# Performance work log

Hardware: AMD Instinct MI355X
Metric: run time of the kernel (lower is better)

## Reference

```python
import jax, jax.numpy as jnp
import numpy as np

DIM = 384
HEADS = 12
W = 7  # window_size
N = W * W
B = 4096

def _relative_position_index(ws):
    ch = np.arange(ws)
    coords = np.stack(np.meshgrid(ch, ch, indexing='ij'))  # [2, W, W]
    cf = coords.reshape(2, -1)  # [2, W*W]
    rel = cf[:, :, None] - cf[:, None, :]  # [2, N, N]
    rel = rel.transpose(1, 2, 0)
    rel[:, :, 0] += ws - 1
    rel[:, :, 1] += ws - 1
    rel[:, :, 0] *= 2 * ws - 1
    return rel.sum(-1).astype(np.int32)  # [N, N]

def setup_inputs() -> dict:
    key = jax.random.key(0)
    ks = jax.random.split(key, 8)
    s = 0.02
    return {
        'x': jax.random.normal(ks[0], (B, N, DIM), jnp.float32),
        'y': jax.random.normal(ks[1], (B, N, DIM), jnp.float32),
        'q_w': jax.random.normal(ks[2], (DIM, DIM), jnp.float32) * s,
        'q_b': jnp.zeros((DIM,), jnp.float32),
        'kv_w': jax.random.normal(ks[3], (2 * DIM, DIM), jnp.float32) * s,
        'kv_b': jnp.zeros((2 * DIM,), jnp.float32),
        'proj_w': jax.random.normal(ks[4], (DIM, DIM), jnp.float32) * s,
        'proj_b': jnp.zeros((DIM,), jnp.float32),
        'rel_table': jax.random.normal(ks[5], ((2 * W - 1) ** 2, HEADS), jnp.float32) * s,
        'rel_index': jnp.asarray(_relative_position_index(W)),
    }

def reference(x, y, q_w, q_b, kv_w, kv_b, proj_w, proj_b, rel_table, rel_index):
    Bx, N1, C = x.shape
    N2 = y.shape[1]
    hd = C // HEADS
    scale = hd ** -0.5
    # projections (torch Linear: x @ W^T + b)
    q = (x @ q_w.T + q_b).reshape(Bx, N1, HEADS, hd)
    kv = (y @ kv_w.T + kv_b).reshape(Bx, N2, 2, HEADS, hd)
    k = kv[:, :, 0]  # [B, N2, H, d]
    v = kv[:, :, 1]
    attn = jnp.einsum('bqhd,bkhd->bhqk', q, k) * scale
    # relative position bias: [N1, N2, H] -> [H, N1, N2]
    bias = rel_table[rel_index.reshape(-1)].reshape(N1, N2, HEADS)
    attn = attn + jnp.transpose(bias, (2, 0, 1))[None]
    attn = jax.nn.softmax(attn, axis=-1)
    out = jnp.einsum('bhqk,bkhd->bqhd', attn, v).reshape(Bx, N1, C)
    return out @ proj_w.T + proj_b
```

## Files before the change

kernel.cpp:

```cpp
#include <hip/hip_runtime.h>

#define DIM 384
#define HEADS 12
#define HD 32
#define NTOK 49
#define NWIN 4096
#define MTOT (NWIN*NTOK)
#define PSTR 72

typedef __attribute__((ext_vector_type(8))) __bf16 bf16x8;
typedef __attribute__((ext_vector_type(4))) float f32x4;

static __device__ __forceinline__ f32x4 mfma16(bf16x8 a, bf16x8 b, f32x4 c) {
  return __builtin_amdgcn_mfma_f32_16x16x32_bf16(a, b, c, 0, 0, 0);
}

static __device__ __forceinline__ void gload_lds16(const void* g, void* l) {
  __builtin_amdgcn_global_load_lds(
      (const __attribute__((address_space(1))) unsigned int*)g,
      (__attribute__((address_space(3))) unsigned int*)l, 16, 0, 0);
}

__global__ void k_prep(const float* __restrict__ qw, const float* __restrict__ kvw,
                       const float* __restrict__ pw, const float* __restrict__ rel_table,
                       const int* __restrict__ rel_index,
                       __bf16* __restrict__ qw_bf, __bf16* __restrict__ kvw_bf,
                       __bf16* __restrict__ pw_bf, float* __restrict__ bias_pad) {
  int i = blockIdx.x * 256 + threadIdx.x;
  if (i < DIM*DIM)   qw_bf[i] = (__bf16)qw[i];
  if (i < 2*DIM*DIM) kvw_bf[i] = (__bf16)kvw[i];
  if (i < DIM*DIM)   pw_bf[i] = (__bf16)pw[i];
  if (i < HEADS*64*64) {
    int h = i >> 12, rem = i & 4095, q = rem >> 6, k = rem & 63;
    float v;
    if (k >= NTOK)      v = -1e30f;
    else if (q >= NTOK) v = 0.0f;
    else v = rel_table[rel_index[q*NTOK + k] * HEADS + h];
    bias_pad[i] = v;
  }
}

__global__ __launch_bounds__(256) void k_qkv(
    const float* __restrict__ x, const float* __restrict__ y,
    const __bf16* __restrict__ qw_bf, const __bf16* __restrict__ kvw_bf,
    const float* __restrict__ q_b, const float* __restrict__ kv_b,
    __bf16* __restrict__ Qws, __bf16* __restrict__ Kws, __bf16* __restrict__ Vws)
{
  int b = blockIdx.x;
  int orig = (b & 7) * 1764 + (b >> 3);
  int mtile = orig / 9;
  int nt9 = orig - mtile*9;
  const float* A; const __bf16* Bw; const float* bias; __bf16* Cout;
  int wrow0, col0;
  if (nt9 < 3) { A = x; Bw = qw_bf; bias = q_b; Cout = Qws; wrow0 = nt9*128; col0 = wrow0; }
  else {
    A = y; Bw = kvw_bf; bias = kv_b; wrow0 = (nt9-3)*128;
    if (wrow0 < DIM) { Cout = Kws; col0 = wrow0; } else { Cout = Vws; col0 = wrow0 - DIM; }
  }
  bias += wrow0;

  __shared__ __align__(16) float  As[2][128*32];
  __shared__ __align__(16) __bf16 Bs[2][128*32];

  int t = threadIdx.x;
  int lane = t & 63, wave = t >> 6;
  int l15 = lane & 15, g = lane >> 4;
  int wr = (wave >> 1) * 64, wc = (wave & 1) * 64;
  int row0b = mtile*128;

  const float* asrc[4];
  #pragma unroll
  for (int i = 0; i < 4; ++i)
    asrc[i] = A + (size_t)(row0b + i*32 + wave*8 + (lane>>3))*DIM
                + (((lane&7) ^ (lane>>3)) << 2);
  const __bf16* bsrc[2];
  #pragma unroll
  for (int i = 0; i < 2; ++i)
    bsrc[i] = Bw + (size_t)(wrow0 + i*64 + wave*16 + (lane>>2))*DIM
                 + (((lane&3) ^ ((lane>>2)&3)) << 3);

  f32x4 acc[4][4];
  #pragma unroll
  for (int a=0;a<4;a++)
    #pragma unroll
    for (int bb=0;bb<4;bb++) acc[a][bb] = (f32x4){0.f,0.f,0.f,0.f};

  #pragma unroll
  for (int i = 0; i < 4; ++i)
    gload_lds16(asrc[i], (char*)&As[0][0] + i*4096 + wave*1024);
  #pragma unroll
  for (int i = 0; i < 2; ++i)
    gload_lds16(bsrc[i], (char*)&Bs[0][0] + i*4096 + wave*1024);
  __syncthreads();

  int buf = 0;
  for (int kt = 0; kt < 12; ++kt) {
    if (kt < 11) {
      int kk = (kt+1)*32;
      #pragma unroll
      for (int i = 0; i < 4; ++i)
        gload_lds16(asrc[i] + kk, (char*)&As[buf^1][0] + i*4096 + wave*1024);
      #pragma unroll
      for (int i = 0; i < 2; ++i)
        gload_lds16(bsrc[i] + kk, (char*)&Bs[buf^1][0] + i*4096 + wave*1024);
    }
    bf16x8 af[4], bfv[4];
    #pragma unroll
    for (int a=0;a<4;a++) {
      int r = wr + a*16 + l15;
      const char* rowp = (const char*)&As[buf][0] + r*128;
      float4 v0 = *(const float4*)(rowp + ((((g<<1)  ) ^ (r&7)) << 4));
      float4 v1 = *(const float4*)(rowp + ((((g<<1)|1) ^ (r&7)) << 4));
      bf16x8 tt;
      tt[0]=(__bf16)v0.x; tt[1]=(__bf16)v0.y; tt[2]=(__bf16)v0.z; tt[3]=(__bf16)v0.w;
      tt[4]=(__bf16)v1.x; tt[5]=(__bf16)v1.y; tt[6]=(__bf16)v1.z; tt[7]=(__bf16)v1.w;
      af[a] = tt;
    }
    #pragma unroll
    for (int bb=0;bb<4;bb++) {
      int r = wc + bb*16 + l15;
      bfv[bb] = *(const bf16x8*)((const char*)&Bs[buf][0] + r*64 + ((g ^ (r&3)) << 4));
    }
    #pragma unroll
    for (int a=0;a<4;a++)
      #pragma unroll
      for (int bb=0;bb<4;bb++)
        acc[a][bb] = mfma16(af[a], bfv[bb], acc[a][bb]);
    __syncthreads();
    buf ^= 1;
  }

  #pragma unroll
  for (int a=0;a<4;a++) {
    #pragma unroll
    for (int bb=0;bb<4;bb++) {
      int colw = wc + bb*16 + l15;
      float bi = bias[colw];
      size_t cbase = (size_t)(row0b + wr + a*16 + 4*g)*DIM + (col0 + colw);
      #pragma unroll
      for (int r=0;r<4;r++)
        Cout[cbase + (size_t)r*DIM] = (__bf16)(acc[a][bb][r] + bi);
    }
  }
}

__global__ __launch_bounds__(256) void k_attn(
    __bf16* qao,
    const __bf16* __restrict__ Kws, const __bf16* __restrict__ Vws,
    const float* __restrict__ bias_pad)
{
  __shared__ __align__(16) __bf16 Psh[4][64*PSTR];
  __shared__ __align__(16) __bf16 VTsh[4][32*PSTR];
  int b = blockIdx.x;
  int lane = threadIdx.x & 63, wave = threadIdx.x >> 6;
  int l15 = lane & 15, g = lane >> 4;
  __bf16* Pw  = Psh[wave];
  __bf16* VTw = VTsh[wave];
  size_t rowbase = (size_t)b * NTOK * DIM;
  const float scale = 0.17677669529663687f;

  for (int e = lane; e < 32*15; e += 64) {
    int d = e / 15, k = 49 + (e - d*15);
    VTw[d*PSTR + k] = (__bf16)0.0f;
  }

  for (int hh = 0; hh < 3; hh++) {
    int h = wave + hh*4;
    for (int e = lane; e < NTOK*HD; e += 64) {
      int k = e >> 5, d = e & 31;
      VTw[d*PSTR + k] = Vws[rowbase + (size_t)k*DIM + h*HD + d];
    }
    bf16x8 qf[4], kf[4];
    #pragma unroll
    for (int mt=0; mt<4; mt++) {
      int q = 16*mt + l15; if (q > 48) q = 48;
      qf[mt] = *(const bf16x8*)(qao + rowbase + (size_t)q*DIM + h*HD + g*8);
    }
    #pragma unroll
    for (int nt=0; nt<4; nt++) {
      int kk = 16*nt + l15; if (kk > 48) kk = 48;
      kf[nt] = *(const bf16x8*)(Kws + rowbase + (size_t)kk*DIM + h*HD + g*8);
    }
    f32x4 sacc[4][4];
    #pragma unroll
    for (int mt=0; mt<4; mt++)
      #pragma unroll
      for (int nt=0; nt<4; nt++)
        sacc[mt][nt] = mfma16(qf[mt], kf[nt], (f32x4){0.f,0.f,0.f,0.f});

    const float* bt = bias_pad + h*4096;
    float rs[4][4];
    #pragma unroll
    for (int mt=0; mt<4; mt++) {
      #pragma unroll
      for (int r=0; r<4; r++) {
        int q = 16*mt + 4*g + r;
        float v0 = sacc[mt][0][r]*scale + bt[q*64 +  0 + l15];
        float v1 = sacc[mt][1][r]*scale + bt[q*64 + 16 + l15];
        float v2 = sacc[mt][2][r]*scale + bt[q*64 + 32 + l15];
        float v3 = sacc[mt][3][r]*scale + bt[q*64 + 48 + l15];
        float m = fmaxf(fmaxf(v0,v1), fmaxf(v2,v3));
        #pragma unroll
        for (int off=1; off<16; off<<=1) m = fmaxf(m, __shfl_xor(m, off));
        v0 = __expf(v0-m); v1 = __expf(v1-m); v2 = __expf(v2-m); v3 = __expf(v3-m);
        float s = v0+v1+v2+v3;
        #pragma unroll
        for (int off=1; off<16; off<<=1) s += __shfl_xor(s, off);
        rs[mt][r] = s;
        Pw[q*PSTR +  0 + l15] = (__bf16)v0;
        Pw[q*PSTR + 16 + l15] = (__bf16)v1;
        Pw[q*PSTR + 32 + l15] = (__bf16)v2;
        Pw[q*PSTR + 48 + l15] = (__bf16)v3;
      }
    }

    #pragma unroll
    for (int mt=0; mt<4; mt++) {
      #pragma unroll
      for (int dt=0; dt<2; dt++) {
        f32x4 o = (f32x4){0.f,0.f,0.f,0.f};
        #pragma unroll
        for (int ks=0; ks<2; ks++) {
          bf16x8 pa = *(const bf16x8*)(Pw  + (16*mt + l15)*PSTR + 32*ks + 8*g);
          bf16x8 vb = *(const bf16x8*)(VTw + (16*dt + l15)*PSTR + 32*ks + 8*g);
          o = mfma16(pa, vb, o);
        }
        #pragma unroll
        for (int r=0; r<4; r++) {
          int q = 16*mt + 4*g + r;
          if (q < NTOK)
            qao[rowbase + (size_t)q*DIM + h*HD + 16*dt + l15] = (__bf16)(o[r] / rs[mt][r]);
        }
      }
    }
  }
}

__global__ __launch_bounds__(256) void k_proj(
    const __bf16* __restrict__ Aao, const __bf16* __restrict__ pw_bf,
    const float* __restrict__ pb, float* __restrict__ out)
{
  int b = blockIdx.x;
  int orig = (b & 7) * 588 + (b >> 3);
  int mtile = orig / 3;
  int nt = orig - mtile*3;
  int lane = threadIdx.x & 63, wave = threadIdx.x >> 6;
  int l15 = lane & 15, g = lane >> 4;
  int wr = (wave >> 1) * 64, wc = (wave & 1) * 64;
  int row0b = mtile*128;
  int col00 = nt*128;

  __shared__ __align__(16) __bf16 As[2][128*32];
  __shared__ __align__(16) __bf16 Bs[2][128*32];

  const __bf16* asrc[2];
  const __bf16* bsrc[2];
  #pragma unroll
  for (int i = 0; i < 2; ++i) {
    asrc[i] = Aao   + (size_t)(row0b + i*64 + wave*16 + (lane>>2))*DIM
                    + (((lane&3) ^ ((lane>>2)&3)) << 3);
    bsrc[i] = pw_bf + (size_t)(col00 + i*64 + wave*16 + (lane>>2))*DIM
                    + (((lane&3) ^ ((lane>>2)&3)) << 3);
  }

  f32x4 acc[4][4];
  #pragma unroll
  for (int a=0;a<4;a++)
    #pragma unroll
    for (int bb=0;bb<4;bb++) acc[a][bb] = (f32x4){0.f,0.f,0.f,0.f};

  #pragma unroll
  for (int i = 0; i < 2; ++i) {
    gload_lds16(asrc[i], (char*)&As[0][0] + i*4096 + wave*1024);
    gload_lds16(bsrc[i], (char*)&Bs[0][0] + i*4096 + wave*1024);
  }
  __syncthreads();

  int buf = 0;
  for (int kt = 0; kt < 12; ++kt) {
    if (kt < 11) {
      int kk = (kt+1)*32;
      #pragma unroll
      for (int i = 0; i < 2; ++i) {
        gload_lds16(asrc[i] + kk, (char*)&As[buf^1][0] + i*4096 + wave*1024);
        gload_lds16(bsrc[i] + kk, (char*)&Bs[buf^1][0] + i*4096 + wave*1024);
      }
    }
    bf16x8 af[4], bfv[4];
    #pragma unroll
    for (int a=0;a<4;a++) {
      int r = wr + a*16 + l15;
      af[a] = *(const bf16x8*)((const char*)&As[buf][0] + r*64 + ((g ^ (r&3)) << 4));
    }
    #pragma unroll
    for (int bb=0;bb<4;bb++) {
      int r = wc + bb*16 + l15;
      bfv[bb] = *(const bf16x8*)((const char*)&Bs[buf][0] + r*64 + ((g ^ (r&3)) << 4));
    }
    #pragma unroll
    for (int a=0;a<4;a++)
      #pragma unroll
      for (int bb=0;bb<4;bb++)
        acc[a][bb] = mfma16(af[a], bfv[bb], acc[a][bb]);
    __syncthreads();
    buf ^= 1;
  }

  #pragma unroll
  for (int a=0;a<4;a++) {
    #pragma unroll
    for (int bb=0;bb<4;bb++) {
      int col = col00 + wc + bb*16 + l15;
      float bi = pb[col];
      size_t cbase = (size_t)(row0b + wr + a*16 + 4*g)*DIM + col;
      #pragma unroll
      for (int r=0;r<4;r++)
        out[cbase + (size_t)r*DIM] = acc[a][bb][r] + bi;
    }
  }
}

extern "C" void kernel_launch(void* const* d_in, const int* in_sizes, int n_in,
                              void* d_out, int out_size, void* d_ws, size_t ws_size,
                              hipStream_t stream)
{
  const float* x   = (const float*)d_in[0];
  const float* y   = (const float*)d_in[1];
  const float* qw  = (const float*)d_in[2];
  const float* qb  = (const float*)d_in[3];
  const float* kvw = (const float*)d_in[4];
  const float* kvb = (const float*)d_in[5];
  const float* pw  = (const float*)d_in[6];
  const float* pb  = (const float*)d_in[7];
  const float* rt  = (const float*)d_in[8];
  const int*   ri  = (const int*)d_in[9];
  float* out = (float*)d_out;

  char* ws = (char*)d_ws;
  const size_t WS_NEEDED = 1376256ull + 3ull*154140672ull;
  if (ws_size < WS_NEEDED) return;

  __bf16* qw_bf    = (__bf16*)(ws);
  __bf16* kvw_bf   = (__bf16*)(ws + 294912);
  __bf16* pw_bf    = (__bf16*)(ws + 884736);
  float*  bias_pad = (float*)(ws + 1179648);
  __bf16* Qws      = (__bf16*)(ws + 1376256);
  __bf16* Kws      = Qws + (size_t)MTOT*DIM;
  __bf16* Vws      = Kws + (size_t)MTOT*DIM;

  k_prep<<<dim3(1152), dim3(256), 0, stream>>>(qw, kvw, pw, rt, ri, qw_bf, kvw_bf, pw_bf, bias_pad);
  k_qkv <<<dim3(1568*9), dim3(256), 0, stream>>>(x, y, qw_bf, kvw_bf, qb, kvb, Qws, Kws, Vws);
  k_attn<<<dim3(NWIN), dim3(256), 0, stream>>>(Qws, Kws, Vws, bias_pad);
  k_proj<<<dim3(1568*3), dim3(256), 0, stream>>>(Qws, pw_bf, pb, out);
}
```

Baseline: 891.3 us.

## Pre-convert activations to bf16 in a separate pass before the QKV GEMM

Adds a streaming kernel that converts x and y from fp32 to bf16 into the output buffer, which is used as scratch. The QKV GEMM then loads bf16 tiles, halving its LDS footprint and dropping the per-tile conversion. Both GEMMs get a new swizzled LDS layout, occupancy hints of 4 blocks per unit and an unroll-2 pragma. The cost is an extra full read of the fp32 inputs plus a bf16 write and reread. Previously each fp32 element was read about 3 times, once per column tile of the GEMM, so the total traffic may still shrink.

```diff
diff --git a/kernel.cpp b/kernel.cpp
--- a/kernel.cpp
+++ b/kernel.cpp
@@ -40,8 +40,27 @@
   }
 }
 
-__global__ __launch_bounds__(256) void k_qkv(
-    const float* __restrict__ x, const float* __restrict__ y,
+__global__ __launch_bounds__(256) void k_cvt(const float* __restrict__ x,
+                                             const float* __restrict__ y,
+                                             __bf16* __restrict__ xb,
+                                             __bf16* __restrict__ yb) {
+  const size_t NCH = (size_t)MTOT * DIM / 8;
+  size_t i = (size_t)blockIdx.x * 256 + threadIdx.x;
+  size_t stride = (size_t)gridDim.x * 256;
+  for (; i < 2*NCH; i += stride) {
+    const float* s; __bf16* d; size_t c;
+    if (i < NCH) { s = x; d = xb; c = i; } else { s = y; d = yb; c = i - NCH; }
+    float4 v0 = *(const float4*)(s + c*8);
+    float4 v1 = *(const float4*)(s + c*8 + 4);
+    bf16x8 t;
+    t[0]=(__bf16)v0.x; t[1]=(__bf16)v0.y; t[2]=(__bf16)v0.z; t[3]=(__bf16)v0.w;
+    t[4]=(__bf16)v1.x; t[5]=(__bf16)v1.y; t[6]=(__bf16)v1.z; t[7]=(__bf16)v1.w;
+    *(bf16x8*)(d + c*8) = t;
+  }
+}
+
+__global__ __launch_bounds__(256, 4) void k_qkv(
+    const __bf16* __restrict__ xb, const __bf16* __restrict__ yb,
     const __bf16* __restrict__ qw_bf, const __bf16* __restrict__ kvw_bf,
     const float* __restrict__ q_b, const float* __restrict__ kv_b,
     __bf16* __restrict__ Qws, __bf16* __restrict__ Kws, __bf16* __restrict__ Vws)
@@ -50,34 +69,32 @@
   int orig = (b & 7) * 1764 + (b >> 3);
   int mtile = orig / 9;
   int nt9 = orig - mtile*9;
-  const float* A; const __bf16* Bw; const float* bias; __bf16* Cout;
+  const __bf16* A; const __bf16* Bw; const float* bias; __bf16* Cout;
   int wrow0, col0;
-  if (nt9 < 3) { A = x; Bw = qw_bf; bias = q_b; Cout = Qws; wrow0 = nt9*128; col0 = wrow0; }
+  if (nt9 < 3) { A = xb; Bw = qw_bf; bias = q_b; Cout = Qws; wrow0 = nt9*128; col0 = wrow0; }
   else {
-    A = y; Bw = kvw_bf; bias = kv_b; wrow0 = (nt9-3)*128;
+    A = yb; Bw = kvw_bf; bias = kv_b; wrow0 = (nt9-3)*128;
     if (wrow0 < DIM) { Cout = Kws; col0 = wrow0; } else { Cout = Vws; col0 = wrow0 - DIM; }
   }
   bias += wrow0;
 
-  __shared__ __align__(16) float  As[2][128*32];
+  __shared__ __align__(16) __bf16 As[2][128*32];
   __shared__ __align__(16) __bf16 Bs[2][128*32];
 
-  int t = threadIdx.x;
-  int lane = t & 63, wave = t >> 6;
+  int t = threadIdx.x, lane = t & 63, wave = t >> 6;
   int l15 = lane & 15, g = lane >> 4;
   int wr = (wave >> 1) * 64, wc = (wave & 1) * 64;
   int row0b = mtile*128;
 
-  const float* asrc[4];
-  #pragma unroll
-  for (int i = 0; i < 4; ++i)
-    asrc[i] = A + (size_t)(row0b + i*32 + wave*8 + (lane>>3))*DIM
-                + (((lane&7) ^ (lane>>3)) << 2);
-  const __bf16* bsrc[2];
-  #pragma unroll
-  for (int i = 0; i < 2; ++i)
-    bsrc[i] = Bw + (size_t)(wrow0 + i*64 + wave*16 + (lane>>2))*DIM
-                 + (((lane&3) ^ ((lane>>2)&3)) << 3);
+  int sr  = 2*(lane >> 3) + ((lane >> 2) & 1);
+  int scb = (lane & 3) ^ ((lane >> 3) & 3);
+  const __bf16* asrc[2]; const __bf16* bsrc[2];
+  #pragma unroll
+  for (int j = 0; j < 2; ++j) {
+    int ar = (wave*2 + j)*16 + sr;
+    asrc[j] = A  + (size_t)(row0b + ar)*DIM + scb*8;
+    bsrc[j] = Bw + (size_t)(wrow0 + ar)*DIM + scb*8;
+  }
 
   f32x4 acc[4][4];
   #pragma unroll
@@ -86,41 +103,32 @@
     for (int bb=0;bb<4;bb++) acc[a][bb] = (f32x4){0.f,0.f,0.f,0.f};
 
   #pragma unroll
-  for (int i = 0; i < 4; ++i)
-    gload_lds16(asrc[i], (char*)&As[0][0] + i*4096 + wave*1024);
-  #pragma unroll
-  for (int i = 0; i < 2; ++i)
-    gload_lds16(bsrc[i], (char*)&Bs[0][0] + i*4096 + wave*1024);
+  for (int j = 0; j < 2; ++j) {
+    gload_lds16(asrc[j], (char*)&As[0][0] + (wave*2+j)*1024);
+    gload_lds16(bsrc[j], (char*)&Bs[0][0] + (wave*2+j)*1024);
+  }
   __syncthreads();
 
+  int lslot = l15*64 + ((g ^ ((l15 >> 1) & 3)) << 4);
+
   int buf = 0;
+  #pragma unroll 2
   for (int kt = 0; kt < 12; ++kt) {
     if (kt < 11) {
       int kk = (kt+1)*32;
       #pragma unroll
-      for (int i = 0; i < 4; ++i)
-        gload_lds16(asrc[i] + kk, (char*)&As[buf^1][0] + i*4096 + wave*1024);
-      #pragma unroll
-      for (int i = 0; i < 2; ++i)
-        gload_lds16(bsrc[i] + kk, (char*)&Bs[buf^1][0] + i*4096 + wave*1024);
+      for (int j = 0; j < 2; ++j) {
+        gload_lds16(asrc[j] + kk, (char*)&As[buf^1][0] + (wave*2+j)*1024);
+        gload_lds16(bsrc[j] + kk, (char*)&Bs[buf^1][0] + (wave*2+j)*1024);
+      }
     }
     bf16x8 af[4], bfv[4];
     #pragma unroll
-    for (int a=0;a<4;a++) {
-      int r = wr + a*16 + l15;
-      const char* rowp = (const char*)&As[buf][0] + r*128;
-      float4 v0 = *(const float4*)(rowp + ((((g<<1)  ) ^ (r&7)) << 4));
-      float4 v1 = *(const float4*)(rowp + ((((g<<1)|1) ^ (r&7)) << 4));
-      bf16x8 tt;
-      tt[0]=(__bf16)v0.x; tt[1]=(__bf16)v0.y; tt[2]=(__bf16)v0.z; tt[3]=(__bf16)v0.w;
-      tt[4]=(__bf16)v1.x; tt[5]=(__bf16)v1.y; tt[6]=(__bf16)v1.z; tt[7]=(__bf16)v1.w;
-      af[a] = tt;
-    }
-    #pragma unroll
-    for (int bb=0;bb<4;bb++) {
-      int r = wc + bb*16 + l15;
-      bfv[bb] = *(const bf16x8*)((const char*)&Bs[buf][0] + r*64 + ((g ^ (r&3)) << 4));
-    }
+    for (int a=0;a<4;a++)
+      af[a]  = *(const bf16x8*)((const char*)&As[buf][0] + (wr + a*16)*64 + lslot);
+    #pragma unroll
+    for (int bb=0;bb<4;bb++)
+      bfv[bb] = *(const bf16x8*)((const char*)&Bs[buf][0] + (wc + bb*16)*64 + lslot);
     #pragma unroll
     for (int a=0;a<4;a++)
       #pragma unroll
@@ -236,7 +244,7 @@
   }
 }
 
-__global__ __launch_bounds__(256) void k_proj(
+__global__ __launch_bounds__(256, 4) void k_proj(
     const __bf16* __restrict__ Aao, const __bf16* __restrict__ pw_bf,
     const float* __restrict__ pb, float* __restrict__ out)
 {
@@ -253,14 +261,14 @@
   __shared__ __align__(16) __bf16 As[2][128*32];
   __shared__ __align__(16) __bf16 Bs[2][128*32];
 
-  const __bf16* asrc[2];
-  const __bf16* bsrc[2];
-  #pragma unroll
-  for (int i = 0; i < 2; ++i) {
-    asrc[i] = Aao   + (size_t)(row0b + i*64 + wave*16 + (lane>>2))*DIM
-                    + (((lane&3) ^ ((lane>>2)&3)) << 3);
-    bsrc[i] = pw_bf + (size_t)(col00 + i*64 + wave*16 + (lane>>2))*DIM
-                    + (((lane&3) ^ ((lane>>2)&3)) << 3);
+  int sr  = 2*(lane >> 3) + ((lane >> 2) & 1);
+  int scb = (lane & 3) ^ ((lane >> 3) & 3);
+  const __bf16* asrc[2]; const __bf16* bsrc[2];
+  #pragma unroll
+  for (int j = 0; j < 2; ++j) {
+    int ar = (wave*2 + j)*16 + sr;
+    asrc[j] = Aao   + (size_t)(row0b + ar)*DIM + scb*8;
+    bsrc[j] = pw_bf + (size_t)(col00 + ar)*DIM + scb*8;
   }
 
   f32x4 acc[4][4];
@@ -270,33 +278,32 @@
     for (int bb=0;bb<4;bb++) acc[a][bb] = (f32x4){0.f,0.f,0.f,0.f};
 
   #pragma unroll
-  for (int i = 0; i < 2; ++i) {
-    gload_lds16(asrc[i], (char*)&As[0][0] + i*4096 + wave*1024);
-    gload_lds16(bsrc[i], (char*)&Bs[0][0] + i*4096 + wave*1024);
+  for (int j = 0; j < 2; ++j) {
+    gload_lds16(asrc[j], (char*)&As[0][0] + (wave*2+j)*1024);
+    gload_lds16(bsrc[j], (char*)&Bs[0][0] + (wave*2+j)*1024);
   }
   __syncthreads();
 
+  int lslot = l15*64 + ((g ^ ((l15 >> 1) & 3)) << 4);
+
   int buf = 0;
+  #pragma unroll 2
   for (int kt = 0; kt < 12; ++kt) {
     if (kt < 11) {
       int kk = (kt+1)*32;
       #pragma unroll
-      for (int i = 0; i < 2; ++i) {
-        gload_lds16(asrc[i] + kk, (char*)&As[buf^1][0] + i*4096 + wave*1024);
-        gload_lds16(bsrc[i] + kk, (char*)&Bs[buf^1][0] + i*4096 + wave*1024);
+      for (int j = 0; j < 2; ++j) {
+        gload_lds16(asrc[j] + kk, (char*)&As[buf^1][0] + (wave*2+j)*1024);
+        gload_lds16(bsrc[j] + kk, (char*)&Bs[buf^1][0] + (wave*2+j)*1024);
       }
     }
     bf16x8 af[4], bfv[4];
     #pragma unroll
-    for (int a=0;a<4;a++) {
-      int r = wr + a*16 + l15;
-      af[a] = *(const bf16x8*)((const char*)&As[buf][0] + r*64 + ((g ^ (r&3)) << 4));
-    }
-    #pragma unroll
-    for (int bb=0;bb<4;bb++) {
-      int r = wc + bb*16 + l15;
-      bfv[bb] = *(const bf16x8*)((const char*)&Bs[buf][0] + r*64 + ((g ^ (r&3)) << 4));
-    }
+    for (int a=0;a<4;a++)
+      af[a]  = *(const bf16x8*)((const char*)&As[buf][0] + (wr + a*16)*64 + lslot);
+    #pragma unroll
+    for (int bb=0;bb<4;bb++)
+      bfv[bb] = *(const bf16x8*)((const char*)&Bs[buf][0] + (wc + bb*16)*64 + lslot);
     #pragma unroll
     for (int a=0;a<4;a++)
       #pragma unroll
@@ -348,8 +355,12 @@
   __bf16* Kws      = Qws + (size_t)MTOT*DIM;
   __bf16* Vws      = Kws + (size_t)MTOT*DIM;
 
+  __bf16* xb = (__bf16*)d_out;
+  __bf16* yb = xb + (size_t)MTOT*DIM;
+
   k_prep<<<dim3(1152), dim3(256), 0, stream>>>(qw, kvw, pw, rt, ri, qw_bf, kvw_bf, pw_bf, bias_pad);
-  k_qkv <<<dim3(1568*9), dim3(256), 0, stream>>>(x, y, qw_bf, kvw_bf, qb, kvb, Qws, Kws, Vws);
+  k_cvt <<<dim3(4096), dim3(256), 0, stream>>>(x, y, xb, yb);
+  k_qkv <<<dim3(1568*9), dim3(256), 0, stream>>>(xb, yb, qw_bf, kvw_bf, qb, kvb, Qws, Kws, Vws);
   k_attn<<<dim3(NWIN), dim3(256), 0, stream>>>(Qws, Kws, Vws, bias_pad);
   k_proj<<<dim3(1568*3), dim3(256), 0, stream>>>(Qws, pw_bf, pb, out);
 }
```

Result: slower. 950.9 us (+6.7%).
